# Optimization experiments

Hardware: AMD Instinct MI355X
Metric: run time of the kernel (lower is better)

Reference implementation:

```python
import jax, jax.numpy as jnp
import numpy as np

V_BOOK, V_AUTH, V_LANG, V_TAG = 10001, 5001, 28, 34253
D = 32  # EMBED_DIM
B, C, LH, LW = 4096, 100, 200, 50


def setup_inputs() -> dict:
    key = jax.random.key(0)
    ks = jax.random.split(key, 32)
    it = iter(ks)

    def emb(k, v):
        t = jax.random.normal(k, (v, D), jnp.float32) * 0.05
        return t.at[0].set(0.0)  # padding_idx=0

    def lin(k, i, o):
        k1, k2 = jax.random.split(k)
        lim = 1.0 / np.sqrt(i)
        return (jax.random.uniform(k1, (i, o), jnp.float32, -lim, lim),
                jax.random.uniform(k2, (o,), jnp.float32, -lim, lim))

    hist = jax.random.randint(next(it), (B, LH), 0, V_BOOK)
    wish = jax.random.randint(next(it), (B, LW), 0, V_BOOK)
    cand = jax.random.randint(next(it), (B, C), 0, V_BOOK)
    auth = jax.random.randint(next(it), (B, C), 0, V_AUTH)
    lang = jax.random.randint(next(it), (B, C), 0, V_LANG)
    tags = jax.random.randint(next(it), (B, C, 5), 0, V_TAG)
    dense = jax.random.normal(next(it), (B, C, 3), jnp.float32)

    E_hist = emb(next(it), V_BOOK)
    E_wish = emb(next(it), V_BOOK)
    E_cand = emb(next(it), V_BOOK)
    E_auth = emb(next(it), V_AUTH)
    E_lang = emb(next(it), V_LANG)
    E_tags = emb(next(it), V_TAG)

    Wb0, bb0 = lin(next(it), 3, 32)
    Wb1, bb1 = lin(next(it), 32, D)
    Wt0, bt0 = lin(next(it), 2 * D, 256)
    Wt1, bt1 = lin(next(it), 256, 128)
    Wt2, bt2 = lin(next(it), 128, 64)
    Wt3, bt3 = lin(next(it), 64, 1)

    return dict(hist=hist, wish=wish, cand=cand, auth=auth, lang=lang, tags=tags,
                dense=dense, E_hist=E_hist, E_wish=E_wish, E_cand=E_cand,
                E_auth=E_auth, E_lang=E_lang, E_tags=E_tags,
                Wb0=Wb0, bb0=bb0, Wb1=Wb1, bb1=bb1,
                Wt0=Wt0, bt0=bt0, Wt1=Wt1, bt1=bt1,
                Wt2=Wt2, bt2=bt2, Wt3=Wt3, bt3=bt3)


def reference(hist, wish, cand, auth, lang, tags, dense,
              E_hist, E_wish, E_cand, E_auth, E_lang, E_tags,
              Wb0, bb0, Wb1, bb1, Wt0, bt0, Wt1, bt1, Wt2, bt2, Wt3, bt3):
    # user side: mean-pooled history + wishlist embeddings  [B, D]
    u_vec = E_hist[hist].mean(axis=1) + E_wish[wish].mean(axis=1)
    # item side: candidate + author + language + mean of 5 tag embeddings  [B, C, D]
    e_t = E_tags[tags].sum(axis=2) / 5.0
    i_vec = E_cand[cand] + E_auth[auth] + E_lang[lang] + e_t
    # bottom MLP on dense features  [B, C, D]
    h = jax.nn.relu(jnp.einsum('bcf,fh->bch', dense, Wb0) + bb0)
    d_vec = jnp.einsum('bch,hd->bcd', h, Wb1) + bb1
    i_final = i_vec + d_vec
    # concat broadcast user vec with item vec  [B, C, 2D]
    u_exp = jnp.broadcast_to(u_vec[:, None, :], (u_vec.shape[0], i_final.shape[1], u_vec.shape[1]))
    x = jnp.concatenate([u_exp, i_final], axis=2)
    # top MLP -> scores [B, C]
    x = jax.nn.relu(x @ Wt0 + bt0)
    x = jax.nn.relu(x @ Wt1 + bt1)
    x = jax.nn.relu(x @ Wt2 + bt2)
    scores = (x @ Wt3 + bt3)[..., 0]
    return scores
```

## Files before the change

kernel.cpp:

```cpp
#include <hip/hip_runtime.h>
#include <hip/hip_bf16.h>
#include <stdint.h>

#define NB 4096
#define NC 100
#define NROWS (NB*NC)
#define NTILES (NROWS/64)
#define GRID_F 768
#define LH 200
#define LW 50

typedef short v8s __attribute__((ext_vector_type(8)));
typedef float v4f __attribute__((ext_vector_type(4)));
typedef float v2f __attribute__((ext_vector_type(2)));
typedef uint32_t v4u __attribute__((ext_vector_type(4)));

__device__ __forceinline__ v4f mfma16(v8s a, v8s b, v4f c) {
  return __builtin_amdgcn_mfma_f32_16x16x32_bf16(a, b, c, 0, 0, 0);
}

__device__ __forceinline__ uint32_t pkbf(float lo, float hi) {
  uint32_t r;
  asm("v_cvt_pk_bf16_f32 %0, %1, %2" : "=v"(r) : "v"(lo), "v"(hi));
  return r;
}

__device__ __forceinline__ uint16_t bf16r(float f) {
  uint32_t u = __builtin_bit_cast(uint32_t, f);
  u = (u + 0x7fffu + ((u >> 16) & 1u)) >> 16;
  return (uint16_t)u;
}

__device__ __forceinline__ int ntli(const int* p) { return __builtin_nontemporal_load(p); }
__device__ __forceinline__ float ntlf(const float* p) { return __builtin_nontemporal_load(p); }

__device__ __forceinline__ void barx() {
  asm volatile("s_waitcnt lgkmcnt(0)" ::: "memory");
  __builtin_amdgcn_s_barrier();
  asm volatile("" ::: "memory");
}

#define OFF_UVB 0
#define OFF_FW  262144

#define FRAG_B1 0
#define FRAG_T0 2
#define FRAG_T1 34
#define FRAG_T2 98
#define NFRAGS 114

__global__ void k_prep(const float* __restrict__ Wb1, const float* __restrict__ Wt0,
                       const float* __restrict__ Wt1, const float* __restrict__ Wt2,
                       uint16_t* __restrict__ fb) {
  int f = blockIdx.x;
  int t = threadIdx.x;
  uint16_t res[2];
  #pragma unroll
  for (int e2 = 0; e2 < 2; ++e2) {
    int e = t * 2 + e2;
    int l = e >> 3, i = e & 7;
    int lr = l & 15, lg = l >> 4;
    float v;
    if (f < FRAG_T0) {
      v = Wb1[(lg * 8 + i) * 32 + 2 * lr + f];
    } else if (f < FRAG_T1) {
      int g = f - FRAG_T0;
      int wv = g >> 3, ch = (g >> 2) & 1, ks = (g >> 1) & 1, p = g & 1;
      int n = ch * 128 + wv * 32 + p * 16 + lr;
      int kl = ks * 32 + lg * 8 + i;
      v = Wt0[kl * 256 + n];
    } else if (f < FRAG_T2) {
      int g = f - FRAG_T1;
      int wv = g >> 4, ch = (g >> 3) & 1, ks = (g >> 1) & 3, p = g & 1;
      int n = wv * 32 + p * 16 + lr;
      int kl = ks * 32 + lg * 8 + i;
      int ok = ch * 128 + (kl & ~31) + ((kl & 31) >> 1) + ((kl & 1) << 4);
      v = Wt1[ok * 128 + n];
    } else {
      int g = f - FRAG_T2;
      int gc = g >> 2, ks = g & 3;
      int n = gc * 16 + lr;
      int kl = ks * 32 + lg * 8 + i;
      int ok = (kl & ~31) + ((kl & 31) >> 1) + ((kl & 1) << 4);
      v = Wt2[ok * 64 + n];
    }
    res[e2] = bf16r(v);
  }
  *(uint32_t*)(fb + (size_t)f * 512 + t * 2) = (uint32_t)res[0] | ((uint32_t)res[1] << 16);
}

__global__ void k_user_bf(const int* __restrict__ hist, const int* __restrict__ wish,
                          const float* __restrict__ Eh, const float* __restrict__ Ew,
                          uint32_t* __restrict__ uvb) {
  int t = threadIdx.x;
  int d2 = t & 15;
  int r = blockIdx.x * 16 + (t >> 4);
  const int* hr = hist + r * LH;
  float sl = 0.f, sh = 0.f;
  #pragma unroll 8
  for (int j = 0; j < LH; ++j) {
    v2f e = *(const v2f*)(Eh + ntli(hr + j) * 32 + 2 * d2);
    sl += e[0]; sh += e[1];
  }
  const int* wr = wish + r * LW;
  float wl = 0.f, wh = 0.f;
  #pragma unroll 5
  for (int j = 0; j < LW; ++j) {
    v2f e = *(const v2f*)(Ew + ntli(wr + j) * 32 + 2 * d2);
    wl += e[0]; wh += e[1];
  }
  uvb[r * 16 + d2] = pkbf(sl * (1.0f/LH) + wl * (1.0f/LW), sh * (1.0f/LH) + wh * (1.0f/LW));
}

#define SM_CONST 0
#define SM_X     2688
#define SM_H     10880
#define SM_ACT1  14976
#define SM_ACT2  14976
#define SM_IDX   47744
#define SM_BYTES 49792

__global__ __launch_bounds__(256, 3)
void k_fused(const int* __restrict__ cand, const int* __restrict__ auth,
             const int* __restrict__ lang, const int* __restrict__ tags,
             const float* __restrict__ dense,
             const float* __restrict__ Ec, const float* __restrict__ Ea,
             const float* __restrict__ El, const float* __restrict__ Et,
             const float* __restrict__ Wb0, const float* __restrict__ bb0,
             const float* __restrict__ bb1, const float* __restrict__ bt0,
             const float* __restrict__ bt1, const float* __restrict__ bt2,
             const float* __restrict__ Wt3, const float* __restrict__ bt3,
             const uint32_t* __restrict__ uvb, const uint16_t* __restrict__ fw,
             float* __restrict__ out) {
  extern __shared__ char sm[];
  const char* fwp = (const char*)fw;
  float* cf = (float*)(sm + SM_CONST);
  const int t = threadIdx.x;
  const int l = t & 63, wv = t >> 6;
  const int lr = l & 15, lg = l >> 4;
  const int q = t & 3, rowl = t >> 2;

  cf[32 + t] = bt0[t];
  if (t < 128) cf[288 + t] = bt1[t];
  if (t < 64)  { cf[416 + t] = bt2[t]; cf[608 + t] = Wt3[t]; }
  if (t < 32)  { cf[t] = bb1[t]; cf[480 + t] = bb0[t]; }
  if (t < 96)  cf[512 + t] = Wb0[t];
  const float bt3v = bt3[0];

  v8s wbl = *(const v8s*)(fwp + (size_t)(FRAG_B1 + 0) * 1024 + l * 16);
  v8s wbh = *(const v8s*)(fwp + (size_t)(FRAG_B1 + 1) * 1024 + l * 16);

  v4u u4;
  float d3x, d3y, d3z;
  int i2a, i2b;
  v2f gc[4], ga[4], gl[4], gt0[4], gt1[4], gt2[4], gt3[4], gt4[4];

  auto ld_uv = [&](int tl) {
    int rr0 = (tl << 6) + rowl;
    int b = rr0 / 100;
    u4 = *(const v4u*)(uvb + b * 16 + q * 4);
    d3x = ntlf(dense + rr0 * 3 + 0);
    d3y = ntlf(dense + rr0 * 3 + 1);
    d3z = ntlf(dense + rr0 * 3 + 2);
  };
  auto ld_idx = [&](int tl) {
    int rr0 = (tl << 6) + rowl;
    int s0 = q * 2;
    i2a = (s0 == 0) ? ntli(cand + rr0) : (s0 == 2) ? ntli(lang + rr0)
        : (s0 == 4) ? ntli(tags + rr0 * 5 + 1) : ntli(tags + rr0 * 5 + 3);
    i2b = (s0 == 0) ? ntli(auth + rr0) : (s0 == 2) ? ntli(tags + rr0 * 5 + 0)
        : (s0 == 4) ? ntli(tags + rr0 * 5 + 2) : ntli(tags + rr0 * 5 + 4);
  };
  auto issue_gathers = [&]() {
    #pragma unroll
    for (int j = 0; j < 4; ++j) {
      int mrow = 16 * wv + lg * 4 + j;
      const int* ip = (const int*)(sm + SM_IDX + mrow * 32);
      int ic = ip[0], ia = ip[1], il = ip[2];
      int x0 = ip[3], x1 = ip[4], x2 = ip[5], x3 = ip[6], x4 = ip[7];
      gc[j]  = *(const v2f*)(Ec + ic * 32 + 2 * lr);
      ga[j]  = *(const v2f*)(Ea + ia * 32 + 2 * lr);
      gl[j]  = *(const v2f*)(El + il * 32 + 2 * lr);
      gt0[j] = *(const v2f*)(Et + x0 * 32 + 2 * lr);
      gt1[j] = *(const v2f*)(Et + x1 * 32 + 2 * lr);
      gt2[j] = *(const v2f*)(Et + x2 * 32 + 2 * lr);
      gt3[j] = *(const v2f*)(Et + x3 * 32 + 2 * lr);
      gt4[j] = *(const v2f*)(Et + x4 * 32 + 2 * lr);
    }
  };

  const int tile0 = blockIdx.x;
  ld_idx(tile0);
  *(int*)(sm + SM_IDX + rowl * 32 + q * 8)     = i2a;
  *(int*)(sm + SM_IDX + rowl * 32 + q * 8 + 4) = i2b;
  barx();
  issue_gathers();
  ld_uv(tile0);
  { int n1 = tile0 + GRID_F; if (n1 > NTILES - 1) n1 = NTILES - 1; ld_idx(n1); }

  for (int tile = tile0; tile < NTILES; tile += GRID_F) {
    const int r0 = tile << 6;

    {
      int xrb = SM_X + rowl * 128;
      int sw  = (rowl & 7) << 4;
      #pragma unroll
      for (int k2 = 0; k2 < 4; ++k2)
        *(uint32_t*)(sm + xrb + ((q * 16 + k2 * 4) ^ sw)) = u4[k2];
      *(int*)(sm + SM_IDX + rowl * 32 + q * 8)     = i2a;
      *(int*)(sm + SM_IDX + rowl * 32 + q * 8 + 4) = i2b;
      const float* bb0l = cf + 480;
      const float* w0a = cf + 512, *w0b = cf + 544, *w0c = cf + 576;
      int hrb = SM_H + rowl * 64;
      int sw3 = (rowl & 3) << 4;
      #pragma unroll
      for (int u2 = 0; u2 < 4; ++u2) {
        int e0 = q * 8 + u2 * 2, e1 = e0 + 1;
        float h0 = fmaxf(bb0l[e0] + d3x * w0a[e0] + d3y * w0b[e0] + d3z * w0c[e0], 0.f);
        float h1 = fmaxf(bb0l[e1] + d3x * w0a[e1] + d3y * w0b[e1] + d3z * w0c[e1], 0.f);
        *(uint32_t*)(sm + hrb + ((q * 16 + u2 * 4) ^ sw3)) = pkbf(h0, h1);
      }
    }
    barx();

    {
      int hrow = 16 * wv + lr;
      v8s ah = *(const v8s*)(sm + SM_H + hrow * 64 + ((lg * 16) ^ ((hrow & 3) << 4)));
      float b0v = cf[2 * lr], b1v = cf[2 * lr + 1];
      v4f dv0 = {b0v, b0v, b0v, b0v};
      v4f dv1 = {b1v, b1v, b1v, b1v};
      dv0 = mfma16(ah, wbl, dv0);
      dv1 = mfma16(ah, wbh, dv1);
      #pragma unroll
      for (int j = 0; j < 4; ++j) {
        int mrow = 16 * wv + lg * 4 + j;
        float s0 = gc[j][0] + ga[j][0] + gl[j][0]
                 + (gt0[j][0] + gt1[j][0] + gt2[j][0] + gt3[j][0] + gt4[j][0]) * 0.2f + dv0[j];
        float s1 = gc[j][1] + ga[j][1] + gl[j][1]
                 + (gt0[j][1] + gt1[j][1] + gt2[j][1] + gt3[j][1] + gt4[j][1]) * 0.2f + dv1[j];
        *(uint32_t*)(sm + SM_X + mrow * 128 + ((64 + 4 * lr) ^ ((mrow & 7) << 4))) = pkbf(s0, s1);
      }
    }
    barx();

    #pragma unroll
    for (int ch = 0; ch < 2; ++ch) {
      v4f a1[2][4];
      #pragma unroll
      for (int p = 0; p < 2; ++p) {
        float bv = cf[32 + ch * 128 + wv * 32 + p * 16 + lr];
        #pragma unroll
        for (int m = 0; m < 4; ++m) a1[p][m] = (v4f){bv, bv, bv, bv};
      }
      #pragma unroll
      for (int ks = 0; ks < 2; ++ks) {
        v8s f0 = *(const v8s*)(fwp + (size_t)(FRAG_T0 + wv * 8 + ch * 4 + ks * 2 + 0) * 1024 + l * 16);
        v8s f1 = *(const v8s*)(fwp + (size_t)(FRAG_T0 + wv * 8 + ch * 4 + ks * 2 + 1) * 1024 + l * 16);
        #pragma unroll
        for (int m = 0; m < 4; ++m) {
          v8s xa = *(const v8s*)(sm + SM_X + (m * 16 + lr) * 128 + ((ks * 64 + lg * 16) ^ ((lr & 7) << 4)));
          a1[0][m] = mfma16(xa, f0, a1[0][m]);
          a1[1][m] = mfma16(xa, f1, a1[1][m]);
        }
      }
      #pragma unroll
      for (int m = 0; m < 4; ++m) {
        #pragma unroll
        for (int j = 0; j < 4; ++j) {
          int row = m * 16 + lg * 4 + j;
          *(uint32_t*)(sm + SM_ACT1 + row * 512 + ((ch * 256 + wv * 64 + 4 * lr) ^ ((row & 7) << 4)))
            = pkbf(fmaxf(a1[0][m][j], 0.f), fmaxf(a1[1][m][j], 0.f));
        }
      }
    }
    barx();

    v4f acc2[2][4];
    #pragma unroll
    for (int p = 0; p < 2; ++p) {
      float bv = cf[288 + wv * 32 + p * 16 + lr];
      #pragma unroll
      for (int m = 0; m < 4; ++m) acc2[p][m] = (v4f){bv, bv, bv, bv};
    }
    #pragma unroll
    for (int ch = 0; ch < 2; ++ch) {
      #pragma unroll
      for (int ks = 0; ks < 4; ++ks) {
        v8s f0 = *(const v8s*)(fwp + (size_t)(FRAG_T1 + wv * 16 + ch * 8 + ks * 2 + 0) * 1024 + l * 16);
        v8s f1 = *(const v8s*)(fwp + (size_t)(FRAG_T1 + wv * 16 + ch * 8 + ks * 2 + 1) * 1024 + l * 16);
        #pragma unroll
        for (int m = 0; m < 4; ++m) {
          v8s aa = *(const v8s*)(sm + SM_ACT1 + (m * 16 + lr) * 512 + ((ch * 256 + ks * 64 + lg * 16) ^ ((lr & 7) << 4)));
          acc2[0][m] = mfma16(aa, f0, acc2[0][m]);
          acc2[1][m] = mfma16(aa, f1, acc2[1][m]);
        }
      }
    }
    barx();

    #pragma unroll
    for (int m = 0; m < 4; ++m) {
      #pragma unroll
      for (int j = 0; j < 4; ++j) {
        int row = m * 16 + lg * 4 + j;
        *(uint32_t*)(sm + SM_ACT2 + row * 256 + ((wv * 64 + 4 * lr) ^ ((row & 7) << 4)))
          = pkbf(fmaxf(acc2[0][m][j], 0.f), fmaxf(acc2[1][m][j], 0.f));
      }
    }
    barx();

    {
      int arow = 16 * wv + lr;
      float bv0 = cf[416 + lr],      bv1 = cf[416 + 16 + lr];
      float bv2 = cf[416 + 32 + lr], bv3 = cf[416 + 48 + lr];
      v4f a3[4] = {{bv0, bv0, bv0, bv0}, {bv1, bv1, bv1, bv1},
                   {bv2, bv2, bv2, bv2}, {bv3, bv3, bv3, bv3}};
      #pragma unroll
      for (int ks = 0; ks < 4; ++ks) {
        v8s aa = *(const v8s*)(sm + SM_ACT2 + arow * 256 + ((ks * 64 + lg * 16) ^ ((arow & 7) << 4)));
        #pragma unroll
        for (int g = 0; g < 4; ++g) {
          v8s fg = *(const v8s*)(fwp + (size_t)(FRAG_T2 + g * 4 + ks) * 1024 + l * 16);
          a3[g] = mfma16(aa, fg, a3[g]);
        }
      }

      int n1 = tile + GRID_F;     if (n1 > NTILES - 1) n1 = NTILES - 1;
      int n2 = tile + 2 * GRID_F; if (n2 > NTILES - 1) n2 = NTILES - 1;
      ld_uv(n1);
      ld_idx(n2);
      issue_gathers();

      float wr0 = cf[608 + lr],      wr1 = cf[608 + 16 + lr];
      float wr2 = cf[608 + 32 + lr], wr3 = cf[608 + 48 + lr];
      float o[4];
      #pragma unroll
      for (int j = 0; j < 4; ++j) {
        o[j] = fmaxf(a3[0][j], 0.f) * wr0 + fmaxf(a3[1][j], 0.f) * wr1
             + fmaxf(a3[2][j], 0.f) * wr2 + fmaxf(a3[3][j], 0.f) * wr3;
        o[j] += __shfl_xor(o[j], 1);
        o[j] += __shfl_xor(o[j], 2);
        o[j] += __shfl_xor(o[j], 4);
        o[j] += __shfl_xor(o[j], 8);
      }
      if (lr == 0) {
        float4 ov = {o[0] + bt3v, o[1] + bt3v, o[2] + bt3v, o[3] + bt3v};
        *(float4*)(out + r0 + wv * 16 + lg * 4) = ov;
      }
    }
    barx();
  }
}

extern "C" void kernel_launch(void* const* d_in, const int* in_sizes, int n_in,
                              void* d_out, int out_size, void* d_ws, size_t ws_size,
                              hipStream_t stream) {
  const int*   hist  = (const int*)d_in[0];
  const int*   wish  = (const int*)d_in[1];
  const int*   cand  = (const int*)d_in[2];
  const int*   auth  = (const int*)d_in[3];
  const int*   lang  = (const int*)d_in[4];
  const int*   tags  = (const int*)d_in[5];
  const float* dense = (const float*)d_in[6];
  const float* Eh    = (const float*)d_in[7];
  const float* Ew    = (const float*)d_in[8];
  const float* Ec    = (const float*)d_in[9];
  const float* Ea    = (const float*)d_in[10];
  const float* El    = (const float*)d_in[11];
  const float* Et    = (const float*)d_in[12];
  const float* Wb0   = (const float*)d_in[13];
  const float* bb0   = (const float*)d_in[14];
  const float* Wb1   = (const float*)d_in[15];
  const float* bb1   = (const float*)d_in[16];
  const float* Wt0   = (const float*)d_in[17];
  const float* bt0   = (const float*)d_in[18];
  const float* Wt1   = (const float*)d_in[19];
  const float* bt1   = (const float*)d_in[20];
  const float* Wt2   = (const float*)d_in[21];
  const float* bt2   = (const float*)d_in[22];
  const float* Wt3   = (const float*)d_in[23];
  const float* bt3   = (const float*)d_in[24];
  char* wsb = (char*)d_ws;
  float* out = (float*)d_out;

  uint32_t* uvb = (uint32_t*)(wsb + OFF_UVB);
  uint16_t* fw  = (uint16_t*)(wsb + OFF_FW);

  (void)hipFuncSetAttribute((const void*)k_fused,
                            hipFuncAttributeMaxDynamicSharedMemorySize, SM_BYTES);

  k_prep<<<NFRAGS, 256, 0, stream>>>(Wb1, Wt0, Wt1, Wt2, fw);
  k_user_bf<<<NB / 16, 256, 0, stream>>>(hist, wish, Eh, Ew, uvb);
  k_fused<<<GRID_F, 256, SM_BYTES, stream>>>(cand, auth, lang, tags, dense,
      Ec, Ea, El, Et, Wb0, bb0, bb1, bt0, bt1, bt2, Wt3, bt3, uvb, fw, out);
}
```

Before: 325.4 us.

## Gather from bf16 copies of item embedding tables and drop cross-tile gather prefetch

Adds a conversion kernel that packs the tag, candidate, author and language embedding tables to bf16 in workspace on every call. The fused kernel then gathers 4-byte bf16 pairs instead of 8-byte float pairs, halving gather traffic. The register-held gather prefetch for the next tile is removed: gathers are now issued inline during the item-vector phase, while only indices, dense and user vectors are prefetched. The trailing loop barrier is also dropped. The trade-offs are extra conversion launches, lost overlap of gather latency with MLP compute, and added bf16 rounding on the embedding values.

```diff
diff --git a/kernel.cpp b/kernel.cpp
--- a/kernel.cpp
+++ b/kernel.cpp
@@ -31,6 +31,9 @@
   return (uint16_t)u;
 }
 
+__device__ __forceinline__ float flo(uint32_t u) { return __builtin_bit_cast(float, u << 16); }
+__device__ __forceinline__ float fhi(uint32_t u) { return __builtin_bit_cast(float, u & 0xffff0000u); }
+
 __device__ __forceinline__ int ntli(const int* p) { return __builtin_nontemporal_load(p); }
 __device__ __forceinline__ float ntlf(const float* p) { return __builtin_nontemporal_load(p); }
 
@@ -42,12 +45,31 @@
 
 #define OFF_UVB 0
 #define OFF_FW  262144
+#define OFF_TB  393216
+#define ET_BYTES (34253*64)
+#define EC_BYTES (10001*64)
+#define EA_BYTES (5001*64)
+#define EL_BYTES (28*64)
+#define WS_ALL (OFF_TB + ET_BYTES + EC_BYTES + EA_BYTES + EL_BYTES)
+#define WS_ET  (OFF_TB + ET_BYTES)
+#define WS_CAL (OFF_TB + EC_BYTES + EA_BYTES + EL_BYTES)
 
 #define FRAG_B1 0
 #define FRAG_T0 2
 #define FRAG_T1 34
 #define FRAG_T2 98
 #define NFRAGS 114
+
+__global__ void k_cvt1(const float* __restrict__ src, uint32_t* __restrict__ dst, int n8) {
+  int i = blockIdx.x * 256 + threadIdx.x;
+  if (i >= n8) return;
+  const float* p = src + (size_t)i * 8;
+  float4 a = *(const float4*)p;
+  float4 b = *(const float4*)(p + 4);
+  uint32_t* d = dst + (size_t)i * 4;
+  d[0] = pkbf(a.x, a.y); d[1] = pkbf(a.z, a.w);
+  d[2] = pkbf(b.x, b.y); d[3] = pkbf(b.z, b.w);
+}
 
 __global__ void k_prep(const float* __restrict__ Wb1, const float* __restrict__ Wt0,
                        const float* __restrict__ Wt1, const float* __restrict__ Wt2,
@@ -112,6 +134,18 @@
   uvb[r * 16 + d2] = pkbf(sl * (1.0f/LH) + wl * (1.0f/LW), sh * (1.0f/LH) + wh * (1.0f/LW));
 }
 
+template<int BF>
+__device__ __forceinline__ void g2t(const uint16_t* B, const float* F, int idx, int lr,
+                                    float& a0, float& a1) {
+  if constexpr (BF) {
+    uint32_t g = *(const uint32_t*)((const char*)B + ((size_t)idx << 6) + (lr << 2));
+    a0 = flo(g); a1 = fhi(g);
+  } else {
+    v2f e = *(const v2f*)(F + idx * 32 + 2 * lr);
+    a0 = e[0]; a1 = e[1];
+  }
+}
+
 #define SM_CONST 0
 #define SM_X     2688
 #define SM_H     10880
@@ -120,12 +154,15 @@
 #define SM_IDX   47744
 #define SM_BYTES 49792
 
+template<int TET, int TEC, int TEA, int TEL>
 __global__ __launch_bounds__(256, 3)
 void k_fused(const int* __restrict__ cand, const int* __restrict__ auth,
              const int* __restrict__ lang, const int* __restrict__ tags,
              const float* __restrict__ dense,
              const float* __restrict__ Ec, const float* __restrict__ Ea,
              const float* __restrict__ El, const float* __restrict__ Et,
+             const uint16_t* __restrict__ EcB, const uint16_t* __restrict__ EaB,
+             const uint16_t* __restrict__ ElB, const uint16_t* __restrict__ EtB,
              const float* __restrict__ Wb0, const float* __restrict__ bb0,
              const float* __restrict__ bb1, const float* __restrict__ bt0,
              const float* __restrict__ bt1, const float* __restrict__ bt2,
@@ -153,52 +190,24 @@
   v4u u4;
   float d3x, d3y, d3z;
   int i2a, i2b;
-  v2f gc[4], ga[4], gl[4], gt0[4], gt1[4], gt2[4], gt3[4], gt4[4];
-
-  auto ld_uv = [&](int tl) {
+  auto ld_tile = [&](int tl) {
     int rr0 = (tl << 6) + rowl;
     int b = rr0 / 100;
     u4 = *(const v4u*)(uvb + b * 16 + q * 4);
     d3x = ntlf(dense + rr0 * 3 + 0);
     d3y = ntlf(dense + rr0 * 3 + 1);
     d3z = ntlf(dense + rr0 * 3 + 2);
-  };
-  auto ld_idx = [&](int tl) {
-    int rr0 = (tl << 6) + rowl;
     int s0 = q * 2;
     i2a = (s0 == 0) ? ntli(cand + rr0) : (s0 == 2) ? ntli(lang + rr0)
         : (s0 == 4) ? ntli(tags + rr0 * 5 + 1) : ntli(tags + rr0 * 5 + 3);
     i2b = (s0 == 0) ? ntli(auth + rr0) : (s0 == 2) ? ntli(tags + rr0 * 5 + 0)
         : (s0 == 4) ? ntli(tags + rr0 * 5 + 2) : ntli(tags + rr0 * 5 + 4);
   };
-  auto issue_gathers = [&]() {
-    #pragma unroll
-    for (int j = 0; j < 4; ++j) {
-      int mrow = 16 * wv + lg * 4 + j;
-      const int* ip = (const int*)(sm + SM_IDX + mrow * 32);
-      int ic = ip[0], ia = ip[1], il = ip[2];
-      int x0 = ip[3], x1 = ip[4], x2 = ip[5], x3 = ip[6], x4 = ip[7];
-      gc[j]  = *(const v2f*)(Ec + ic * 32 + 2 * lr);
-      ga[j]  = *(const v2f*)(Ea + ia * 32 + 2 * lr);
-      gl[j]  = *(const v2f*)(El + il * 32 + 2 * lr);
-      gt0[j] = *(const v2f*)(Et + x0 * 32 + 2 * lr);
-      gt1[j] = *(const v2f*)(Et + x1 * 32 + 2 * lr);
-      gt2[j] = *(const v2f*)(Et + x2 * 32 + 2 * lr);
-      gt3[j] = *(const v2f*)(Et + x3 * 32 + 2 * lr);
-      gt4[j] = *(const v2f*)(Et + x4 * 32 + 2 * lr);
-    }
-  };
-
-  const int tile0 = blockIdx.x;
-  ld_idx(tile0);
-  *(int*)(sm + SM_IDX + rowl * 32 + q * 8)     = i2a;
-  *(int*)(sm + SM_IDX + rowl * 32 + q * 8 + 4) = i2b;
+  ld_tile(blockIdx.x);
+
   barx();
-  issue_gathers();
-  ld_uv(tile0);
-  { int n1 = tile0 + GRID_F; if (n1 > NTILES - 1) n1 = NTILES - 1; ld_idx(n1); }
-
-  for (int tile = tile0; tile < NTILES; tile += GRID_F) {
+
+  for (int tile = blockIdx.x; tile < NTILES; tile += GRID_F) {
     const int r0 = tile << 6;
 
     {
@@ -234,14 +243,26 @@
       #pragma unroll
       for (int j = 0; j < 4; ++j) {
         int mrow = 16 * wv + lg * 4 + j;
-        float s0 = gc[j][0] + ga[j][0] + gl[j][0]
-                 + (gt0[j][0] + gt1[j][0] + gt2[j][0] + gt3[j][0] + gt4[j][0]) * 0.2f + dv0[j];
-        float s1 = gc[j][1] + ga[j][1] + gl[j][1]
-                 + (gt0[j][1] + gt1[j][1] + gt2[j][1] + gt3[j][1] + gt4[j][1]) * 0.2f + dv1[j];
+        const int* ip = (const int*)(sm + SM_IDX + mrow * 32);
+        int ic = ip[0], ia = ip[1], il = ip[2];
+        int x0 = ip[3], x1 = ip[4], x2 = ip[5], x3 = ip[6], x4 = ip[7];
+        float c0, c1, a0, a1, l0, l1, p0, p1, p2, p3, p4, p5, p6, p7, p8, p9;
+        g2t<TEC>(EcB, Ec, ic, lr, c0, c1);
+        g2t<TEA>(EaB, Ea, ia, lr, a0, a1);
+        g2t<TEL>(ElB, El, il, lr, l0, l1);
+        g2t<TET>(EtB, Et, x0, lr, p0, p1);
+        g2t<TET>(EtB, Et, x1, lr, p2, p3);
+        g2t<TET>(EtB, Et, x2, lr, p4, p5);
+        g2t<TET>(EtB, Et, x3, lr, p6, p7);
+        g2t<TET>(EtB, Et, x4, lr, p8, p9);
+        float s0 = c0 + a0 + l0 + (p0 + p2 + p4 + p6 + p8) * 0.2f + dv0[j];
+        float s1 = c1 + a1 + l1 + (p1 + p3 + p5 + p7 + p9) * 0.2f + dv1[j];
         *(uint32_t*)(sm + SM_X + mrow * 128 + ((64 + 4 * lr) ^ ((mrow & 7) << 4))) = pkbf(s0, s1);
       }
     }
     barx();
+
+    if (tile + GRID_F < NTILES) ld_tile(tile + GRID_F);
 
     #pragma unroll
     for (int ch = 0; ch < 2; ++ch) {
@@ -324,13 +345,6 @@
           a3[g] = mfma16(aa, fg, a3[g]);
         }
       }
-
-      int n1 = tile + GRID_F;     if (n1 > NTILES - 1) n1 = NTILES - 1;
-      int n2 = tile + 2 * GRID_F; if (n2 > NTILES - 1) n2 = NTILES - 1;
-      ld_uv(n1);
-      ld_idx(n2);
-      issue_gathers();
-
       float wr0 = cf[608 + lr],      wr1 = cf[608 + 16 + lr];
       float wr2 = cf[608 + 32 + lr], wr3 = cf[608 + 48 + lr];
       float o[4];
@@ -348,8 +362,25 @@
         *(float4*)(out + r0 + wv * 16 + lg * 4) = ov;
       }
     }
-    barx();
-  }
+  }
+}
+
+template<int TET, int TEC, int TEA, int TEL>
+static void launch_fused(const int* cand, const int* auth, const int* lang, const int* tags,
+                         const float* dense, const float* Ec, const float* Ea,
+                         const float* El, const float* Et,
+                         const uint16_t* EcB, const uint16_t* EaB,
+                         const uint16_t* ElB, const uint16_t* EtB,
+                         const float* Wb0, const float* bb0, const float* bb1,
+                         const float* bt0, const float* bt1, const float* bt2,
+                         const float* Wt3, const float* bt3,
+                         const uint32_t* uvb, const uint16_t* fw, float* out,
+                         hipStream_t stream) {
+  auto kf = k_fused<TET, TEC, TEA, TEL>;
+  (void)hipFuncSetAttribute((const void*)kf, hipFuncAttributeMaxDynamicSharedMemorySize, SM_BYTES);
+  kf<<<GRID_F, 256, SM_BYTES, stream>>>(cand, auth, lang, tags, dense,
+      Ec, Ea, El, Et, EcB, EaB, ElB, EtB, Wb0, bb0, bb1, bt0, bt1, bt2, Wt3, bt3,
+      uvb, fw, out);
 }
 
 extern "C" void kernel_launch(void* const* d_in, const int* in_sizes, int n_in,
@@ -386,11 +417,40 @@
   uint32_t* uvb = (uint32_t*)(wsb + OFF_UVB);
   uint16_t* fw  = (uint16_t*)(wsb + OFF_FW);
 
-  (void)hipFuncSetAttribute((const void*)k_fused,
-                            hipFuncAttributeMaxDynamicSharedMemorySize, SM_BYTES);
-
   k_prep<<<NFRAGS, 256, 0, stream>>>(Wb1, Wt0, Wt1, Wt2, fw);
   k_user_bf<<<NB / 16, 256, 0, stream>>>(hist, wish, Eh, Ew, uvb);
-  k_fused<<<GRID_F, 256, SM_BYTES, stream>>>(cand, auth, lang, tags, dense,
-      Ec, Ea, El, Et, Wb0, bb0, bb1, bt0, bt1, bt2, Wt3, bt3, uvb, fw, out);
-}
+
+  if (ws_size >= (size_t)WS_ALL) {
+    uint16_t* EtB = (uint16_t*)(wsb + OFF_TB);
+    uint16_t* EcB = (uint16_t*)(wsb + OFF_TB + ET_BYTES);
+    uint16_t* EaB = (uint16_t*)(wsb + OFF_TB + ET_BYTES + EC_BYTES);
+    uint16_t* ElB = (uint16_t*)(wsb + OFF_TB + ET_BYTES + EC_BYTES + EA_BYTES);
+    k_cvt1<<<(34253*4 + 255)/256, 256, 0, stream>>>(Et, (uint32_t*)EtB, 34253*4);
+    k_cvt1<<<(10001*4 + 255)/256, 256, 0, stream>>>(Ec, (uint32_t*)EcB, 10001*4);
+    k_cvt1<<<(5001*4 + 255)/256, 256, 0, stream>>>(Ea, (uint32_t*)EaB, 5001*4);
+    k_cvt1<<<1, 256, 0, stream>>>(El, (uint32_t*)ElB, 28*4);
+    launch_fused<1,1,1,1>(cand, auth, lang, tags, dense, Ec, Ea, El, Et,
+                          EcB, EaB, ElB, EtB, Wb0, bb0, bb1, bt0, bt1, bt2, Wt3, bt3,
+                          uvb, fw, out, stream);
+  } else if (ws_size >= (size_t)WS_ET) {
+    uint16_t* EtB = (uint16_t*)(wsb + OFF_TB);
+    k_cvt1<<<(34253*4 + 255)/256, 256, 0, stream>>>(Et, (uint32_t*)EtB, 34253*4);
+    launch_fused<1,0,0,0>(cand, auth, lang, tags, dense, Ec, Ea, El, Et,
+                          nullptr, nullptr, nullptr, EtB, Wb0, bb0, bb1, bt0, bt1, bt2, Wt3, bt3,
+                          uvb, fw, out, stream);
+  } else if (ws_size >= (size_t)WS_CAL) {
+    uint16_t* EcB = (uint16_t*)(wsb + OFF_TB);
+    uint16_t* EaB = (uint16_t*)(wsb + OFF_TB + EC_BYTES);
+    uint16_t* ElB = (uint16_t*)(wsb + OFF_TB + EC_BYTES + EA_BYTES);
+    k_cvt1<<<(10001*4 + 255)/256, 256, 0, stream>>>(Ec, (uint32_t*)EcB, 10001*4);
+    k_cvt1<<<(5001*4 + 255)/256, 256, 0, stream>>>(Ea, (uint32_t*)EaB, 5001*4);
+    k_cvt1<<<1, 256, 0, stream>>>(El, (uint32_t*)ElB, 28*4);
+    launch_fused<0,1,1,1>(cand, auth, lang, tags, dense, Ec, Ea, El, Et,
+                          EcB, EaB, ElB, nullptr, Wb0, bb0, bb1, bt0, bt1, bt2, Wt3, bt3,
+                          uvb, fw, out, stream);
+  } else {
+    launch_fused<0,0,0,0>(cand, auth, lang, tags, dense, Ec, Ea, El, Et,
+                          nullptr, nullptr, nullptr, nullptr, Wb0, bb0, bb1, bt0, bt1, bt2, Wt3, bt3,
+                          uvb, fw, out, stream);
+  }
+}
```

After: 289.2 us. 1.13x faster.
